# Performance work log

Measured on AMD Instinct MI355X. Metric: run time of the kernel, lower is better.

The kernel has to match this reference:

```python
import jax, jax.numpy as jnp
import numpy as np

BS, N, XC, K, YS = 64, 1024, 1024, 256, 768

def setup_inputs() -> dict:
    key = jax.random.key(0)
    ks = jax.random.split(key, 5)
    return {
        "x": jax.random.normal(ks[0], (BS, N, XC), dtype=jnp.float32),
        "y": jax.random.normal(ks[1], (BS, YS), dtype=jnp.float32),
        "W_ch": jax.random.normal(ks[2], (K, XC), dtype=jnp.float32) * 0.02,
        "b_ch": jax.random.normal(ks[3], (K,), dtype=jnp.float32) * 0.02,
        "W_y": jax.random.normal(ks[4], (K, YS), dtype=jnp.float32) * 0.02,
    }

def reference(x, y, W_ch, b_ch, W_y):
    # y_k: [bs, k] (no bias)
    y_k = jnp.einsum('bs,ks->bk', y, W_y)
    # channel affine on every spatial position, batched: [bs, n, k]
    x_k = jnp.einsum('bnc,kc->bnk', x, W_ch) + b_ch
    # add per-sample y_k (broadcast over spatial dim), tanh, softmax over k
    z = jnp.tanh(x_k + y_k[:, None, :])
    attn = jax.nn.softmax(z, axis=-1)
    # torch.cat over dim=0 of per-sample [n, k] blocks -> [bs*n, k]
    return attn.reshape(-1, attn.shape[-1])
```

## Files before the change

kernel.cpp:

```cpp
#include <hip/hip_runtime.h>


#define XC    1024
#define KOUT  256
#define NT    16
#define A_OFF 65536
#define LDSZ  81920

typedef float        f32x4_t  __attribute__((ext_vector_type(4)));
typedef unsigned int u32x4_t  __attribute__((ext_vector_type(4)));
typedef unsigned int u32x2_t  __attribute__((ext_vector_type(2)));
typedef __bf16       bf16x8_t __attribute__((ext_vector_type(8)));

__device__ __forceinline__ unsigned short f2bf(float f) {
  unsigned int u = __float_as_uint(f);
  u += 0x7fffu + ((u >> 16) & 1u);
  return (unsigned short)(u >> 16);
}

__device__ __forceinline__ float fast_tanh(float v) {
  float e = __expf(2.0f * v);
  return 1.0f - 2.0f / (e + 1.0f);
}

__device__ __forceinline__ void async_copy16(void* lds, const void* g) {
  __builtin_amdgcn_global_load_lds(
      (const __attribute__((address_space(1))) void*)g,
      (__attribute__((address_space(3))) void*)lds, 16, 0, 0);
}

__global__ void wcvt_kernel(const float* __restrict__ Wch,
                            unsigned short* __restrict__ wbf) {
  const int k = blockIdx.x;
  const int t = threadIdx.x;
  f32x4_t v = ((const f32x4_t*)(Wch + k * XC))[t];
  const int tile = t >> 4;
  const int c4   = t & 15;
  unsigned int lo = (unsigned int)f2bf(v.x) | ((unsigned int)f2bf(v.y) << 16);
  unsigned int hi = (unsigned int)f2bf(v.z) | ((unsigned int)f2bf(v.w) << 16);
  char* p = (char*)wbf + tile * 32768 + k * 128 +
            (((c4 >> 1) ^ (k & 7)) << 4) + ((c4 & 1) << 3);
  *(u32x2_t*)p = (u32x2_t){lo, hi};
}

__global__ void bias_kernel(const float* __restrict__ y,
                            const float* __restrict__ Wy,
                            const float* __restrict__ bch,
                            float* __restrict__ biasws) {
  __shared__ __align__(16) float ys[768];
  const int b = blockIdx.x;
  const int k = threadIdx.x;
  for (int i = k; i < 768; i += 256) ys[i] = y[b * 768 + i];
  __syncthreads();
  const f32x4_t* w4 = (const f32x4_t*)(Wy + k * 768);
  const f32x4_t* y4 = (const f32x4_t*)ys;
  float s = 0.f;
#pragma unroll 8
  for (int i = 0; i < 192; ++i) {
    f32x4_t w = w4[i], a = y4[i];
    s = fmaf(w.x, a.x, s); s = fmaf(w.y, a.y, s);
    s = fmaf(w.z, a.z, s); s = fmaf(w.w, a.w, s);
  }
  biasws[b * 256 + k] = s + bch[k];
}

__global__ __launch_bounds__(256, 2) void fused_kernel(
    const float* __restrict__ x, const unsigned short* __restrict__ wbf,
    const float* __restrict__ bias, float* __restrict__ out) {
  __shared__ __align__(16) unsigned char smem[LDSZ];
  const int tid = threadIdx.x;
  const int l   = tid & 63;
  const int wv  = tid >> 6;
  const int lr  = l & 15;
  const int lg  = l >> 4;
  const int m0  = blockIdx.x << 6;
  const int bidx = m0 >> 10;
  const int rr  = tid >> 4;
  const int c4  = tid & 15;

  f32x4_t acc[4][4];
#pragma unroll
  for (int i = 0; i < 4; ++i)
#pragma unroll
    for (int j = 0; j < 4; ++j) acc[i][j] = (f32x4_t){0.f, 0.f, 0.f, 0.f};

  const float* xb = x + (size_t)m0 * XC + (size_t)rr * XC + (c4 << 2);
  f32x4_t av[4];
  const char* wsrc = (const char*)wbf;

  auto loadA = [&](int t) {
#pragma unroll
    for (int j = 0; j < 4; ++j)
      av[j] = *(const f32x4_t*)(xb + (size_t)(j << 4) * XC + (t << 6));
  };
  auto issueB = [&](int t, int buf) {
    const char* g = wsrc + t * 32768 + (wv << 13) + (l << 4);
    unsigned char* d = smem + (buf << 15) + (wv << 13);
#pragma unroll
    for (int i = 0; i < 8; ++i)
      async_copy16(d + (i << 10), g + (i << 10));
  };
  auto writeA = [&](int buf) {
#pragma unroll
    for (int j = 0; j < 4; ++j) {
      const int row = (j << 4) + rr;
      unsigned int lo = (unsigned int)f2bf(av[j].x) | ((unsigned int)f2bf(av[j].y) << 16);
      unsigned int hi = (unsigned int)f2bf(av[j].z) | ((unsigned int)f2bf(av[j].w) << 16);
      char* p = (char*)smem + A_OFF + (buf << 13) + row * 128 +
                (((c4 >> 1) ^ (row & 7)) << 4) + ((c4 & 1) << 3);
      *(u32x2_t*)p = (u32x2_t){lo, hi};
    }
  };
  auto compute = [&](int buf) {
    const u32x4_t* aB = (const u32x4_t*)(smem + A_OFF + (buf << 13));
    const u32x4_t* bB = (const u32x4_t*)(smem + (buf << 15));
#pragma unroll
    for (int kk = 0; kk < 2; ++kk) {
      const int cs = ((kk << 2) | lg) ^ (lr & 7);
      bf16x8_t afr[4], bfr[4];
#pragma unroll
      for (int mi = 0; mi < 4; ++mi)
        afr[mi] = __builtin_bit_cast(bf16x8_t, aB[(((mi << 4) + lr) << 3) + cs]);
#pragma unroll
      for (int ni = 0; ni < 4; ++ni)
        bfr[ni] = __builtin_bit_cast(bf16x8_t,
                    bB[(((wv << 6) + (ni << 4) + lr) << 3) + cs]);
#pragma unroll
      for (int mi = 0; mi < 4; ++mi)
#pragma unroll
        for (int ni = 0; ni < 4; ++ni)
          acc[mi][ni] = __builtin_amdgcn_mfma_f32_16x16x32_bf16(
              afr[mi], bfr[ni], acc[mi][ni], 0, 0, 0);
    }
  };

  loadA(0);
  issueB(0, 0);
  writeA(0);
  __syncthreads();

  for (int t = 0; t < NT; ++t) {
    const int cur = t & 1;
    if (t + 1 < NT) {
      loadA(t + 1);
      issueB(t + 1, cur ^ 1);
    }
    compute(cur);
    if (t + 1 < NT) {
      writeA(cur ^ 1);
      __syncthreads();
    }
  }
  __syncthreads();

  float* wred    = (float*)smem;
  float* rowstat = (float*)(smem + 1024);

  float brow[4];
#pragma unroll
  for (int ni = 0; ni < 4; ++ni)
    brow[ni] = bias[(bidx << 8) + (wv << 6) + (ni << 4) + lr];

#pragma unroll
  for (int mi = 0; mi < 4; ++mi)
#pragma unroll
    for (int ni = 0; ni < 4; ++ni)
#pragma unroll
      for (int r = 0; r < 4; ++r)
        acc[mi][ni][r] = fast_tanh(acc[mi][ni][r] + brow[ni]);

#pragma unroll
  for (int mi = 0; mi < 4; ++mi)
#pragma unroll
    for (int r = 0; r < 4; ++r) {
      float m = fmaxf(fmaxf(acc[mi][0][r], acc[mi][1][r]),
                      fmaxf(acc[mi][2][r], acc[mi][3][r]));
      m = fmaxf(m, __shfl_xor(m, 1));
      m = fmaxf(m, __shfl_xor(m, 2));
      m = fmaxf(m, __shfl_xor(m, 4));
      m = fmaxf(m, __shfl_xor(m, 8));
      if (lr == 0) wred[(wv << 6) + (mi << 4) + (lg << 2) + r] = m;
    }
  __syncthreads();
  if (tid < 64)
    rowstat[tid] = fmaxf(fmaxf(wred[tid], wred[64 + tid]),
                         fmaxf(wred[128 + tid], wred[192 + tid]));
  __syncthreads();

#pragma unroll
  for (int mi = 0; mi < 4; ++mi)
#pragma unroll
    for (int r = 0; r < 4; ++r) {
      const int row = (mi << 4) + (lg << 2) + r;
      const float m = rowstat[row];
      float s = 0.f;
#pragma unroll
      for (int ni = 0; ni < 4; ++ni) {
        float e = __expf(acc[mi][ni][r] - m);
        acc[mi][ni][r] = e;
        s += e;
      }
      s += __shfl_xor(s, 1);
      s += __shfl_xor(s, 2);
      s += __shfl_xor(s, 4);
      s += __shfl_xor(s, 8);
      if (lr == 0) wred[(wv << 6) + row] = s;
    }
  __syncthreads();
  if (tid < 64)
    rowstat[tid] = 1.0f / (wred[tid] + wred[64 + tid] +
                           wred[128 + tid] + wred[192 + tid]);
  __syncthreads();

#pragma unroll
  for (int mi = 0; mi < 4; ++mi)
#pragma unroll
    for (int r = 0; r < 4; ++r) {
      const int row = (mi << 4) + (lg << 2) + r;
      const float rinv = rowstat[row];
      float* orow = out + (size_t)(m0 + row) * KOUT + (wv << 6) + lr;
#pragma unroll
      for (int ni = 0; ni < 4; ++ni)
        orow[ni << 4] = acc[mi][ni][r] * rinv;
    }
}

extern "C" void kernel_launch(void* const* d_in, const int* in_sizes, int n_in,
                              void* d_out, int out_size, void* d_ws, size_t ws_size,
                              hipStream_t stream) {
  (void)in_sizes; (void)n_in; (void)out_size; (void)ws_size;
  const float* x   = (const float*)d_in[0];
  const float* y   = (const float*)d_in[1];
  const float* Wch = (const float*)d_in[2];
  const float* bch = (const float*)d_in[3];
  const float* Wy  = (const float*)d_in[4];
  float* out = (float*)d_out;
  unsigned short* wbf = (unsigned short*)d_ws;
  float* biasws = (float*)((char*)d_ws + 512 * 1024);

  hipLaunchKernelGGL(wcvt_kernel, dim3(256), dim3(256), 0, stream, Wch, wbf);
  hipLaunchKernelGGL(bias_kernel, dim3(64), dim3(256), 0, stream, y, Wy, bch, biasws);
  hipLaunchKernelGGL(fused_kernel, dim3(1024), dim3(256), 0, stream, x, wbf, biasws, out);
}
```

Before: 132.5 us.

## Load bf16 weight fragments directly to registers and merge prep kernels

The weight tile is no longer staged through LDS. It is pre-swizzled into MFMA fragment order so each wave loads its B fragments straight from global memory (L2) into registers. LDS shrinks to a double-buffered A tile, which lifts occupancy limits, and the main loop is unrolled by two with explicit register double-buffering of the x loads and lgkmcnt-only barriers. The weight-conversion and bias kernels are merged into one launch to save a kernel launch. The trade-off is more global/L2 traffic for the weights, since every block re-reads them, and higher register pressure from eight B fragments plus two A staging buffers.

New measurement: 117.5 us. -11.3%, faster.

```diff
diff --git a/kernel.cpp b/kernel.cpp
--- a/kernel.cpp
+++ b/kernel.cpp
@@ -4,8 +4,7 @@
 #define XC    1024
 #define KOUT  256
 #define NT    16
-#define A_OFF 65536
-#define LDSZ  81920
+#define LDSZ  16384
 
 typedef float        f32x4_t  __attribute__((ext_vector_type(4)));
 typedef unsigned int u32x4_t  __attribute__((ext_vector_type(4)));
@@ -23,45 +22,55 @@
   return 1.0f - 2.0f / (e + 1.0f);
 }
 
-__device__ __forceinline__ void async_copy16(void* lds, const void* g) {
-  __builtin_amdgcn_global_load_lds(
-      (const __attribute__((address_space(1))) void*)g,
-      (__attribute__((address_space(3))) void*)lds, 16, 0, 0);
-}
-
-__global__ void wcvt_kernel(const float* __restrict__ Wch,
-                            unsigned short* __restrict__ wbf) {
-  const int k = blockIdx.x;
-  const int t = threadIdx.x;
-  f32x4_t v = ((const f32x4_t*)(Wch + k * XC))[t];
-  const int tile = t >> 4;
-  const int c4   = t & 15;
-  unsigned int lo = (unsigned int)f2bf(v.x) | ((unsigned int)f2bf(v.y) << 16);
-  unsigned int hi = (unsigned int)f2bf(v.z) | ((unsigned int)f2bf(v.w) << 16);
-  char* p = (char*)wbf + tile * 32768 + k * 128 +
-            (((c4 >> 1) ^ (k & 7)) << 4) + ((c4 & 1) << 3);
-  *(u32x2_t*)p = (u32x2_t){lo, hi};
-}
-
-__global__ void bias_kernel(const float* __restrict__ y,
+#define LGKM_BARRIER() do {                                  \
+    asm volatile("s_waitcnt lgkmcnt(0)" ::: "memory");       \
+    __builtin_amdgcn_s_barrier();                            \
+    __builtin_amdgcn_sched_barrier(0);                       \
+  } while (0)
+
+__global__ void prep_kernel(const float* __restrict__ Wch,
+                            const float* __restrict__ y,
                             const float* __restrict__ Wy,
                             const float* __restrict__ bch,
+                            unsigned short* __restrict__ wbf,
                             float* __restrict__ biasws) {
-  __shared__ __align__(16) float ys[768];
-  const int b = blockIdx.x;
-  const int k = threadIdx.x;
-  for (int i = k; i < 768; i += 256) ys[i] = y[b * 768 + i];
-  __syncthreads();
-  const f32x4_t* w4 = (const f32x4_t*)(Wy + k * 768);
-  const f32x4_t* y4 = (const f32x4_t*)ys;
-  float s = 0.f;
+  if (blockIdx.x < 256) {
+    const int k = blockIdx.x;
+    const int u = threadIdx.x;
+    f32x4_t v = ((const f32x4_t*)(Wch + k * XC))[u];
+    const int c0   = u << 2;
+    const int t    = c0 >> 6;
+    const int ch   = (c0 & 63) >> 3;
+    const int kk   = ch >> 2;
+    const int lg   = ch & 3;
+    const int half = (c0 >> 2) & 1;
+    const int wv   = k >> 6;
+    const int ni   = (k >> 4) & 3;
+    const int lr   = k & 15;
+    const int lane = (lg << 4) | lr;
+    unsigned int lo = (unsigned int)f2bf(v.x) | ((unsigned int)f2bf(v.y) << 16);
+    unsigned int hi = (unsigned int)f2bf(v.z) | ((unsigned int)f2bf(v.w) << 16);
+    char* p = (char*)wbf +
+              ((size_t)((((t << 2) + wv) * 2 + kk) * 4 + ni) << 10) +
+              (lane << 4) + (half << 3);
+    *(u32x2_t*)p = (u32x2_t){lo, hi};
+  } else {
+    __shared__ __align__(16) float ys[768];
+    const int b = blockIdx.x - 256;
+    const int k = threadIdx.x;
+    for (int i = k; i < 768; i += 256) ys[i] = y[b * 768 + i];
+    __syncthreads();
+    const f32x4_t* w4 = (const f32x4_t*)(Wy + k * 768);
+    const f32x4_t* y4 = (const f32x4_t*)ys;
+    float s = 0.f;
 #pragma unroll 8
-  for (int i = 0; i < 192; ++i) {
-    f32x4_t w = w4[i], a = y4[i];
-    s = fmaf(w.x, a.x, s); s = fmaf(w.y, a.y, s);
-    s = fmaf(w.z, a.z, s); s = fmaf(w.w, a.w, s);
+    for (int i = 0; i < 192; ++i) {
+      f32x4_t w = w4[i], a = y4[i];
+      s = fmaf(w.x, a.x, s); s = fmaf(w.y, a.y, s);
+      s = fmaf(w.z, a.z, s); s = fmaf(w.w, a.w, s);
+    }
+    biasws[b * 256 + k] = s + bch[k];
   }
-  biasws[b * 256 + k] = s + bch[k];
 }
 
 __global__ __launch_bounds__(256, 2) void fused_kernel(
@@ -85,73 +94,79 @@
     for (int j = 0; j < 4; ++j) acc[i][j] = (f32x4_t){0.f, 0.f, 0.f, 0.f};
 
   const float* xb = x + (size_t)m0 * XC + (size_t)rr * XC + (c4 << 2);
-  f32x4_t av[4];
   const char* wsrc = (const char*)wbf;
-
-  auto loadA = [&](int t) {
-#pragma unroll
-    for (int j = 0; j < 4; ++j)
-      av[j] = *(const f32x4_t*)(xb + (size_t)(j << 4) * XC + (t << 6));
-  };
-  auto issueB = [&](int t, int buf) {
-    const char* g = wsrc + t * 32768 + (wv << 13) + (l << 4);
-    unsigned char* d = smem + (buf << 15) + (wv << 13);
-#pragma unroll
-    for (int i = 0; i < 8; ++i)
-      async_copy16(d + (i << 10), g + (i << 10));
-  };
-  auto writeA = [&](int buf) {
-#pragma unroll
-    for (int j = 0; j < 4; ++j) {
-      const int row = (j << 4) + rr;
-      unsigned int lo = (unsigned int)f2bf(av[j].x) | ((unsigned int)f2bf(av[j].y) << 16);
-      unsigned int hi = (unsigned int)f2bf(av[j].z) | ((unsigned int)f2bf(av[j].w) << 16);
-      char* p = (char*)smem + A_OFF + (buf << 13) + row * 128 +
-                (((c4 >> 1) ^ (row & 7)) << 4) + ((c4 & 1) << 3);
-      *(u32x2_t*)p = (u32x2_t){lo, hi};
-    }
-  };
-  auto compute = [&](int buf) {
-    const u32x4_t* aB = (const u32x4_t*)(smem + A_OFF + (buf << 13));
-    const u32x4_t* bB = (const u32x4_t*)(smem + (buf << 15));
-#pragma unroll
-    for (int kk = 0; kk < 2; ++kk) {
-      const int cs = ((kk << 2) | lg) ^ (lr & 7);
-      bf16x8_t afr[4], bfr[4];
-#pragma unroll
-      for (int mi = 0; mi < 4; ++mi)
-        afr[mi] = __builtin_bit_cast(bf16x8_t, aB[(((mi << 4) + lr) << 3) + cs]);
-#pragma unroll
-      for (int ni = 0; ni < 4; ++ni)
-        bfr[ni] = __builtin_bit_cast(bf16x8_t,
-                    bB[(((wv << 6) + (ni << 4) + lr) << 3) + cs]);
-#pragma unroll
-      for (int mi = 0; mi < 4; ++mi)
-#pragma unroll
-        for (int ni = 0; ni < 4; ++ni)
-          acc[mi][ni] = __builtin_amdgcn_mfma_f32_16x16x32_bf16(
-              afr[mi], bfr[ni], acc[mi][ni], 0, 0, 0);
-    }
-  };
-
-  loadA(0);
-  issueB(0, 0);
-  writeA(0);
-  __syncthreads();
-
-  for (int t = 0; t < NT; ++t) {
-    const int cur = t & 1;
-    if (t + 1 < NT) {
-      loadA(t + 1);
-      issueB(t + 1, cur ^ 1);
-    }
-    compute(cur);
-    if (t + 1 < NT) {
-      writeA(cur ^ 1);
-      __syncthreads();
-    }
+  f32x4_t avA[4], avB[4];
+  bf16x8_t bfr[8];
+
+#define LOADA(dst, tt) do {                                                  \
+    _Pragma("unroll")                                                        \
+    for (int j = 0; j < 4; ++j)                                              \
+      dst[j] = *(const f32x4_t*)(xb + (size_t)(j << 4) * XC + ((tt) << 6));  \
+  } while (0)
+
+#define LOADB(tt) do {                                                       \
+    const char* g = wsrc + (size_t)(tt) * 32768 + (wv << 13) + (l << 4);     \
+    _Pragma("unroll")                                                        \
+    for (int f = 0; f < 8; ++f)                                              \
+      bfr[f] = __builtin_bit_cast(bf16x8_t, *(const u32x4_t*)(g + (f << 10)));\
+  } while (0)
+
+#define WRITEA(src, buf) do {                                                \
+    _Pragma("unroll")                                                        \
+    for (int j = 0; j < 4; ++j) {                                            \
+      const int row = (j << 4) + rr;                                         \
+      unsigned int lo = (unsigned int)f2bf(src[j].x) |                       \
+                        ((unsigned int)f2bf(src[j].y) << 16);                \
+      unsigned int hi = (unsigned int)f2bf(src[j].z) |                       \
+                        ((unsigned int)f2bf(src[j].w) << 16);                \
+      char* p = (char*)smem + ((buf) << 13) + row * 128 +                    \
+                (((c4 >> 1) ^ (row & 7)) << 4) + ((c4 & 1) << 3);            \
+      *(u32x2_t*)p = (u32x2_t){lo, hi};                                      \
+    }                                                                        \
+  } while (0)
+
+#define COMPUTE(buf) do {                                                    \
+    const u32x4_t* aB = (const u32x4_t*)(smem + ((buf) << 13));              \
+    _Pragma("unroll")                                                        \
+    for (int kk = 0; kk < 2; ++kk) {                                         \
+      const int cs = ((kk << 2) | lg) ^ (lr & 7);                            \
+      bf16x8_t afr[4];                                                       \
+      _Pragma("unroll")                                                      \
+      for (int mi = 0; mi < 4; ++mi)                                         \
+        afr[mi] = __builtin_bit_cast(bf16x8_t, aB[(((mi << 4) + lr) << 3) + cs]);\
+      _Pragma("unroll")                                                      \
+      for (int mi = 0; mi < 4; ++mi)                                         \
+        _Pragma("unroll")                                                    \
+        for (int nj = 0; nj < 4; ++nj)                                       \
+          acc[mi][nj] = __builtin_amdgcn_mfma_f32_16x16x32_bf16(             \
+              afr[mi], bfr[(kk << 2) | nj], acc[mi][nj], 0, 0, 0);           \
+    }                                                                        \
+  } while (0)
+
+  LOADA(avA, 0);
+  LOADA(avB, 1);
+  LOADB(0);
+  WRITEA(avA, 0);
+  LGKM_BARRIER();
+
+  for (int t = 0; t < NT; t += 2) {
+    if (t + 2 < NT) LOADA(avA, t + 2);
+    COMPUTE(0);
+    if (t + 1 < NT) LOADB(t + 1);
+    if (t + 1 < NT) WRITEA(avB, 1);
+    LGKM_BARRIER();
+    if (t + 3 < NT) LOADA(avB, t + 3);
+    COMPUTE(1);
+    if (t + 2 < NT) LOADB(t + 2);
+    if (t + 2 < NT) WRITEA(avA, 0);
+    if (t + 2 < NT) LGKM_BARRIER();
   }
   __syncthreads();
+
+#undef LOADA
+#undef LOADB
+#undef WRITEA
+#undef COMPUTE
 
   float* wred    = (float*)smem;
   float* rowstat = (float*)(smem + 1024);
@@ -238,7 +253,8 @@
   unsigned short* wbf = (unsigned short*)d_ws;
   float* biasws = (float*)((char*)d_ws + 512 * 1024);
 
-  hipLaunchKernelGGL(wcvt_kernel, dim3(256), dim3(256), 0, stream, Wch, wbf);
-  hipLaunchKernelGGL(bias_kernel, dim3(64), dim3(256), 0, stream, y, Wy, bch, biasws);
-  hipLaunchKernelGGL(fused_kernel, dim3(1024), dim3(256), 0, stream, x, wbf, biasws, out);
-}
+  hipLaunchKernelGGL(prep_kernel, dim3(320), dim3(256), 0, stream,
+                     Wch, y, Wy, bch, wbf, biasws);
+  hipLaunchKernelGGL(fused_kernel, dim3(1024), dim3(256), 0, stream,
+                     x, wbf, biasws, out);
+}
```
